# Optimization experiments

Hardware: AMD Instinct MI355X
Metric: run time of the kernel (lower is better)

Reference implementation:

```python
import jax, jax.numpy as jnp
import numpy as np

N_NODES = 50000


def gcn_conv(x, edge_index, W, b, n_nodes):
    # Linear transform first (as in PyG GCNConv), then normalized aggregation
    xw = x @ W  # [N, out]
    src, dst = edge_index[0], edge_index[1]
    loops = jnp.arange(n_nodes, dtype=src.dtype)
    s = jnp.concatenate([src, loops])  # add self-loops
    d = jnp.concatenate([dst, loops])
    deg = jax.ops.segment_sum(jnp.ones_like(s, dtype=xw.dtype), d, num_segments=n_nodes)
    dinv = jnp.where(deg > 0, jax.lax.rsqrt(deg), 0.0)
    norm = dinv[s] * dinv[d]  # [E+N]
    msg = xw[s] * norm[:, None]  # gather + scale
    out = jax.ops.segment_sum(msg, d, num_segments=n_nodes)  # scatter-add
    return out + b


def setup_inputs() -> dict:
    key = jax.random.key(0)
    k1, k2, k3, k4 = jax.random.split(key, 4)
    in_dim, hidden = 128, 128
    n_edges = 625000
    x = jax.random.normal(k1, (N_NODES, in_dim), dtype=jnp.float32)
    edge_index = jax.random.randint(k2, (2, n_edges), 0, N_NODES, dtype=jnp.int64)
    # glorot-ish scale
    W1 = jax.random.normal(k3, (in_dim, hidden), dtype=jnp.float32) * (1.0 / np.sqrt(in_dim))
    b1 = jnp.zeros((hidden,), dtype=jnp.float32)
    W2 = jax.random.normal(k4, (hidden, hidden), dtype=jnp.float32) * (1.0 / np.sqrt(hidden))
    b2 = jnp.zeros((hidden,), dtype=jnp.float32)
    return {"x": x, "edge_index": edge_index, "W1": W1, "b1": b1, "W2": W2, "b2": b2}


def reference(x, edge_index, W1, b1, W2, b2):
    n = x.shape[0]
    h = gcn_conv(x, edge_index, W1, b1, n)
    h = jax.nn.relu(h)
    # dropout(p=0.3) is identity in eval mode
    h = gcn_conv(h, edge_index, W2, b2, n)
    return jax.nn.relu(h)
```

## Files before the change

### kernel.cpp

```cpp
#include <hip/hip_runtime.h>
#include <hip/hip_bf16.h>

#define NNODES 50000
#define BKT 64
#define LP 136

typedef short bf16x8 __attribute__((ext_vector_type(8)));
typedef float f32x4 __attribute__((ext_vector_type(4)));

__device__ __forceinline__ unsigned short f2bf_rn(float f) {
    unsigned int u = __float_as_uint(f);
    return (unsigned short)((u + 0x7fffu + ((u >> 16) & 1u)) >> 16);
}
__device__ __forceinline__ float bf_lo(unsigned int u) { return __uint_as_float(u << 16); }
__device__ __forceinline__ float bf_hi(unsigned int u) { return __uint_as_float(u & 0xffff0000u); }

__device__ __forceinline__ void acc8(float* a, uint4 u, float wv) {
    a[0] = fmaf(bf_lo(u.x), wv, a[0]);  a[1] = fmaf(bf_hi(u.x), wv, a[1]);
    a[2] = fmaf(bf_lo(u.y), wv, a[2]);  a[3] = fmaf(bf_hi(u.y), wv, a[3]);
    a[4] = fmaf(bf_lo(u.z), wv, a[4]);  a[5] = fmaf(bf_hi(u.z), wv, a[5]);
    a[6] = fmaf(bf_lo(u.w), wv, a[6]);  a[7] = fmaf(bf_hi(u.w), wv, a[7]);
}


__global__ __launch_bounds__(256) void k_wt(const float* __restrict__ W1,
                                            const float* __restrict__ W2,
                                            unsigned short* __restrict__ WT1,
                                            unsigned short* __restrict__ WT2,
                                            int* __restrict__ cnt, int N) {
    __shared__ float tile[128 * 129];
    int b = blockIdx.x, t = threadIdx.x;
    if (b < 2) {
        const float* W = b ? W2 : W1;
        unsigned short* WT = b ? WT2 : WT1;
        for (int idx = t; idx < 128 * 128; idx += 256)
            tile[(idx >> 7) * 129 + (idx & 127)] = W[idx];
        __syncthreads();
        for (int idx = t; idx < 128 * 128; idx += 256) {
            int c = idx >> 7, k = idx & 127;
            WT[c * 128 + k] = f2bf_rn(tile[k * 129 + c]);
        }
    } else {
        int i = (b - 2) * 256 + t;
        if (i < N) cnt[i] = 0;
    }
}


__global__ __launch_bounds__(256) void k_gemmbucket(const float* __restrict__ X,
                                                    const unsigned short* __restrict__ WT,
                                                    unsigned short* __restrict__ Yb, int n,
                                                    const int* __restrict__ src,
                                                    const int* __restrict__ dst,
                                                    int* __restrict__ cnt,
                                                    unsigned short* __restrict__ bkt,
                                                    int E, int EB) {
    __shared__ unsigned short Wl[128 * LP];
    int t = threadIdx.x;
    if ((int)blockIdx.x < EB) {
        int e = blockIdx.x * 256 + t;
        if (e < E) {
            int s = src[e], d = dst[e];
            int pos = atomicAdd(&cnt[d], 1);
            if (pos < BKT) bkt[(size_t)d * BKT + pos] = (unsigned short)s;
        }
        return;
    }
    int gb = blockIdx.x - EB;
    int lane = t & 63, w = t >> 6;
    int m = lane & 15, quad = lane >> 4;
    int base = gb * 64 + w * 16;
    int row = min(base + m, n - 1);

    bf16x8 a[4];
#pragma unroll
    for (int kt = 0; kt < 4; ++kt) {
        const float* pa = &X[(size_t)row * 128 + kt * 32 + quad * 8];
        float4 v0 = *(const float4*)pa;
        float4 v1 = *(const float4*)(pa + 4);
        a[kt][0] = (short)f2bf_rn(v0.x); a[kt][1] = (short)f2bf_rn(v0.y);
        a[kt][2] = (short)f2bf_rn(v0.z); a[kt][3] = (short)f2bf_rn(v0.w);
        a[kt][4] = (short)f2bf_rn(v1.x); a[kt][5] = (short)f2bf_rn(v1.y);
        a[kt][6] = (short)f2bf_rn(v1.z); a[kt][7] = (short)f2bf_rn(v1.w);
    }
    for (int idx = t; idx < 128 * 16; idx += 256) {
        int r = idx >> 4, c8 = (idx & 15) << 3;
        *(uint4*)&Wl[r * LP + c8] = *(const uint4*)&WT[r * 128 + c8];
    }
    __syncthreads();

    f32x4 acc[8];
#pragma unroll
    for (int i = 0; i < 8; ++i) acc[i] = f32x4{0.f, 0.f, 0.f, 0.f};
#pragma unroll
    for (int kt = 0; kt < 4; ++kt) {
        int ko = kt * 32 + quad * 8;
#pragma unroll
        for (int ct = 0; ct < 8; ++ct) {
            bf16x8 bb = *(const bf16x8*)&Wl[(ct * 16 + m) * LP + ko];
            acc[ct] = __builtin_amdgcn_mfma_f32_16x16x32_bf16(a[kt], bb, acc[ct], 0, 0, 0);
        }
    }
    __syncthreads();

    unsigned short* ep = &Wl[w * 16 * LP];
#pragma unroll
    for (int ct = 0; ct < 8; ++ct)
#pragma unroll
        for (int r = 0; r < 4; ++r)
            ep[(quad * 4 + r) * LP + ct * 16 + m] = f2bf_rn(acc[ct][r]);
    __syncthreads();
    int rr = lane & 15, cc = lane >> 4;
    int orow = base + rr;
    if (orow < n) {
#pragma unroll
        for (int i2 = 0; i2 < 4; ++i2)
            ((uint4*)&Yb[(size_t)orow * 128])[cc * 4 + i2] =
                *(const uint4*)&ep[rr * LP + (cc * 4 + i2) * 8];
    }
}


__global__ __launch_bounds__(1024, 2) void k_aggemm(const unsigned int* __restrict__ xw1u,
                                                    const int* __restrict__ cnt,
                                                    const unsigned short* __restrict__ bkt,
                                                    const float* __restrict__ bias,
                                                    const unsigned short* __restrict__ WT2,
                                                    unsigned short* __restrict__ xw2, int n) {
    __shared__ unsigned short Wl[128 * LP];
    __shared__ unsigned short At[64 * LP];
    int t = threadIdx.x, lane = t & 63, w = t >> 6;
    int base = blockIdx.x * 64;

    for (int idx = t; idx < 128 * 16; idx += 1024) {
        int r = idx >> 4, c8 = (idx & 15) << 3;
        *(uint4*)&Wl[r * LP + c8] = *(const uint4*)&WT2[r * 128 + c8];
    }

    int g = lane >> 4, li = lane & 15;
    int node = min(base + w * 4 + g, n - 1);
    int deg = cnt[node], degc = min(deg, BKT);
    float di = rsqrtf((float)deg + 1.0f);
    uint4 v = *(const uint4*)&xw1u[(size_t)node * 64 + li * 4];
    float a[8];
    a[0] = di * bf_lo(v.x);  a[1] = di * bf_hi(v.x);
    a[2] = di * bf_lo(v.y);  a[3] = di * bf_hi(v.y);
    a[4] = di * bf_lo(v.z);  a[5] = di * bf_hi(v.z);
    a[6] = di * bf_lo(v.w);  a[7] = di * bf_hi(v.w);
    const unsigned short* bp = &bkt[(size_t)node * BKT];
    for (int j = 0; __any(j < degc); j += 8) {
        if (j < degc) {
            uint4 q = *(const uint4*)&bp[j];
            int s0 = q.x & 0xffff, s1 = q.x >> 16, s2 = q.y & 0xffff, s3 = q.y >> 16;
            int s4 = q.z & 0xffff, s5 = q.z >> 16, s6 = q.w & 0xffff, s7 = q.w >> 16;
            uint4 u0 = *(const uint4*)&xw1u[(size_t)s0 * 64 + li * 4];
            uint4 u1 = *(const uint4*)&xw1u[(size_t)s1 * 64 + li * 4];
            uint4 u2 = *(const uint4*)&xw1u[(size_t)s2 * 64 + li * 4];
            uint4 u3 = *(const uint4*)&xw1u[(size_t)s3 * 64 + li * 4];
            uint4 u4 = *(const uint4*)&xw1u[(size_t)s4 * 64 + li * 4];
            uint4 u5 = *(const uint4*)&xw1u[(size_t)s5 * 64 + li * 4];
            uint4 u6 = *(const uint4*)&xw1u[(size_t)s6 * 64 + li * 4];
            uint4 u7 = *(const uint4*)&xw1u[(size_t)s7 * 64 + li * 4];
            float w0 = (j + 0 < degc) ? rsqrtf((float)cnt[s0] + 1.0f) : 0.0f;
            float w1 = (j + 1 < degc) ? rsqrtf((float)cnt[s1] + 1.0f) : 0.0f;
            float w2 = (j + 2 < degc) ? rsqrtf((float)cnt[s2] + 1.0f) : 0.0f;
            float w3 = (j + 3 < degc) ? rsqrtf((float)cnt[s3] + 1.0f) : 0.0f;
            float w4 = (j + 4 < degc) ? rsqrtf((float)cnt[s4] + 1.0f) : 0.0f;
            float w5 = (j + 5 < degc) ? rsqrtf((float)cnt[s5] + 1.0f) : 0.0f;
            float w6 = (j + 6 < degc) ? rsqrtf((float)cnt[s6] + 1.0f) : 0.0f;
            float w7 = (j + 7 < degc) ? rsqrtf((float)cnt[s7] + 1.0f) : 0.0f;
            acc8(a, u0, w0); acc8(a, u1, w1); acc8(a, u2, w2); acc8(a, u3, w3);
            acc8(a, u4, w4); acc8(a, u5, w5); acc8(a, u6, w6); acc8(a, u7, w7);
        }
    }
    float4 b0 = ((const float4*)bias)[li * 2];
    float4 b1v = ((const float4*)bias)[li * 2 + 1];
    float h0 = fmaxf(fmaf(di, a[0], b0.x), 0.f), h1 = fmaxf(fmaf(di, a[1], b0.y), 0.f);
    float h2 = fmaxf(fmaf(di, a[2], b0.z), 0.f), h3 = fmaxf(fmaf(di, a[3], b0.w), 0.f);
    float h4 = fmaxf(fmaf(di, a[4], b1v.x), 0.f), h5 = fmaxf(fmaf(di, a[5], b1v.y), 0.f);
    float h6 = fmaxf(fmaf(di, a[6], b1v.z), 0.f), h7 = fmaxf(fmaf(di, a[7], b1v.w), 0.f);
    uint4 hp;
    hp.x = (unsigned)f2bf_rn(h0) | ((unsigned)f2bf_rn(h1) << 16);
    hp.y = (unsigned)f2bf_rn(h2) | ((unsigned)f2bf_rn(h3) << 16);
    hp.z = (unsigned)f2bf_rn(h4) | ((unsigned)f2bf_rn(h5) << 16);
    hp.w = (unsigned)f2bf_rn(h6) | ((unsigned)f2bf_rn(h7) << 16);
    *(uint4*)&At[(w * 4 + g) * LP + li * 8] = hp;

    int m = lane & 15, quad = lane >> 4;
    int ct = w & 7, mt2 = (w >> 3) * 2;
    float die[2][4];
#pragma unroll
    for (int mt = 0; mt < 2; ++mt)
#pragma unroll
        for (int r = 0; r < 4; ++r)
            die[mt][r] = rsqrtf(
                (float)cnt[min(base + (mt2 + mt) * 16 + quad * 4 + r, n - 1)] + 1.0f);
    __syncthreads();

    f32x4 acc0 = f32x4{0.f, 0.f, 0.f, 0.f};
    f32x4 acc1 = f32x4{0.f, 0.f, 0.f, 0.f};
#pragma unroll
    for (int kt = 0; kt < 4; ++kt) {
        int ko = kt * 32 + quad * 8;
        bf16x8 bb = *(const bf16x8*)&Wl[(ct * 16 + m) * LP + ko];
        bf16x8 aA = *(const bf16x8*)&At[(mt2 * 16 + m) * LP + ko];
        bf16x8 aB = *(const bf16x8*)&At[((mt2 + 1) * 16 + m) * LP + ko];
        acc0 = __builtin_amdgcn_mfma_f32_16x16x32_bf16(aA, bb, acc0, 0, 0, 0);
        acc1 = __builtin_amdgcn_mfma_f32_16x16x32_bf16(aB, bb, acc1, 0, 0, 0);
    }
    __syncthreads();
#pragma unroll
    for (int r = 0; r < 4; ++r) {
        At[(mt2 * 16 + quad * 4 + r) * LP + ct * 16 + m] = f2bf_rn(acc0[r] * die[0][r]);
        At[((mt2 + 1) * 16 + quad * 4 + r) * LP + ct * 16 + m] = f2bf_rn(acc1[r] * die[1][r]);
    }
    __syncthreads();
    {
        int rowi = t >> 4, q = t & 15;
        int orow = base + rowi;
        if (orow < n)
            *(uint4*)&xw2[(size_t)orow * 128 + q * 8] = *(const uint4*)&At[rowi * LP + q * 8];
    }
}


__global__ __launch_bounds__(256) void k_agg(const unsigned int* __restrict__ xw2u,
                                             const int* __restrict__ cnt,
                                             const unsigned short* __restrict__ bkt,
                                             const float* __restrict__ bias,
                                             float* __restrict__ out, int n) {
    int t = threadIdx.x, lane = t & 63, w = t >> 6;
    int g = lane >> 4, li = lane & 15;
    int node = blockIdx.x * 16 + w * 4 + g;
    int nc = min(node, n - 1);
    int deg = cnt[nc], degc = min(deg, BKT);
    float di = rsqrtf((float)deg + 1.0f);
    uint4 v = *(const uint4*)&xw2u[(size_t)nc * 64 + li * 4];
    float a[8];
    a[0] = bf_lo(v.x);  a[1] = bf_hi(v.x);
    a[2] = bf_lo(v.y);  a[3] = bf_hi(v.y);
    a[4] = bf_lo(v.z);  a[5] = bf_hi(v.z);
    a[6] = bf_lo(v.w);  a[7] = bf_hi(v.w);
    const unsigned short* bp = &bkt[(size_t)nc * BKT];
    for (int j = 0; __any(j < degc); j += 8) {
        if (j < degc) {
            uint4 q = *(const uint4*)&bp[j];
            int s0 = q.x & 0xffff, s1 = q.x >> 16, s2 = q.y & 0xffff, s3 = q.y >> 16;
            int s4 = q.z & 0xffff, s5 = q.z >> 16, s6 = q.w & 0xffff, s7 = q.w >> 16;
            uint4 u0 = *(const uint4*)&xw2u[(size_t)s0 * 64 + li * 4];
            uint4 u1 = *(const uint4*)&xw2u[(size_t)s1 * 64 + li * 4];
            uint4 u2 = *(const uint4*)&xw2u[(size_t)s2 * 64 + li * 4];
            uint4 u3 = *(const uint4*)&xw2u[(size_t)s3 * 64 + li * 4];
            uint4 u4 = *(const uint4*)&xw2u[(size_t)s4 * 64 + li * 4];
            uint4 u5 = *(const uint4*)&xw2u[(size_t)s5 * 64 + li * 4];
            uint4 u6 = *(const uint4*)&xw2u[(size_t)s6 * 64 + li * 4];
            uint4 u7 = *(const uint4*)&xw2u[(size_t)s7 * 64 + li * 4];
            float w0 = (j + 0 < degc) ? 1.0f : 0.0f, w1 = (j + 1 < degc) ? 1.0f : 0.0f;
            float w2 = (j + 2 < degc) ? 1.0f : 0.0f, w3 = (j + 3 < degc) ? 1.0f : 0.0f;
            float w4 = (j + 4 < degc) ? 1.0f : 0.0f, w5 = (j + 5 < degc) ? 1.0f : 0.0f;
            float w6 = (j + 6 < degc) ? 1.0f : 0.0f, w7 = (j + 7 < degc) ? 1.0f : 0.0f;
            acc8(a, u0, w0); acc8(a, u1, w1); acc8(a, u2, w2); acc8(a, u3, w3);
            acc8(a, u4, w4); acc8(a, u5, w5); acc8(a, u6, w6); acc8(a, u7, w7);
        }
    }
    float4 b0 = ((const float4*)bias)[li * 2];
    float4 b1v = ((const float4*)bias)[li * 2 + 1];
    float4 o0, o1;
    o0.x = fmaxf(fmaf(di, a[0], b0.x), 0.f);  o0.y = fmaxf(fmaf(di, a[1], b0.y), 0.f);
    o0.z = fmaxf(fmaf(di, a[2], b0.z), 0.f);  o0.w = fmaxf(fmaf(di, a[3], b0.w), 0.f);
    o1.x = fmaxf(fmaf(di, a[4], b1v.x), 0.f); o1.y = fmaxf(fmaf(di, a[5], b1v.y), 0.f);
    o1.z = fmaxf(fmaf(di, a[6], b1v.z), 0.f); o1.w = fmaxf(fmaf(di, a[7], b1v.w), 0.f);
    if (node < n) {
        *(float4*)&out[(size_t)node * 128 + li * 8] = o0;
        *(float4*)&out[(size_t)node * 128 + li * 8 + 4] = o1;
    }
}


extern "C" void kernel_launch(void* const* d_in, const int* in_sizes, int n_in,
                              void* d_out, int out_size, void* d_ws, size_t ws_size,
                              hipStream_t stream) {
    const float* x  = (const float*)d_in[0];
    const int*   ei = (const int*)d_in[1];
    const float* W1 = (const float*)d_in[2];
    const float* b1 = (const float*)d_in[3];
    const float* W2 = (const float*)d_in[4];
    const float* b2 = (const float*)d_in[5];
    float* out = (float*)d_out;

    const int N = NNODES;
    const int E = in_sizes[1] / 2;
    const int* src = ei;
    const int* dst = ei + E;

    char* p = (char*)d_ws;
    size_t off = 0;
    auto take = [&](size_t bytes) -> void* {
        void* r = p + off;
        off = (off + bytes + 255) & ~(size_t)255;
        return r;
    };
    int* cnt = (int*)take((size_t)N * 4);
    unsigned short* bkt = (unsigned short*)take((size_t)N * BKT * 2);
    unsigned short* w1t = (unsigned short*)take(128 * 128 * 2);
    unsigned short* w2t = (unsigned short*)take(128 * 128 * 2);
    unsigned short* xw1 = (unsigned short*)take((size_t)N * 128 * 2);
    unsigned short* xw2 = (unsigned short*)take((size_t)N * 128 * 2);

    const int NB = (N + 255) / 256;
    const int EB = (E + 255) / 256;
    const int GB = (N + 63) / 64;
    const int AB = (N + 15) / 16;

    k_wt<<<2 + NB, 256, 0, stream>>>(W1, W2, w1t, w2t, cnt, N);
    k_gemmbucket<<<EB + GB, 256, 0, stream>>>(x, w1t, xw1, N, src, dst, cnt, bkt, E, EB);
    k_aggemm<<<GB, 1024, 0, stream>>>((const unsigned int*)xw1, cnt, bkt, b1, w2t, xw2, N);
    k_agg<<<AB, 256, 0, stream>>>((const unsigned int*)xw2, cnt, bkt, b2, out, N);
}
```

Before: 209.5 us.

## Shard edge bucketing per XCD and compact buckets with precomputed dinv

Edge bucketing now writes into eight per-XCD sub-buckets indexed by the hardware XCC_ID, so atomics on a node's counter stay within one die's L2 and avoid cross-die contention. A new compaction kernel merges the sub-buckets into the per-node bucket and precomputes the inverse square-root degree once per node. The aggregation kernels then read dinv directly instead of recomputing rsqrt from counts. This adds a kernel launch, a larger zero-init, and extra memory traffic for the 8x counter and bucket arrays.

After: 209.1 us. Within noise of the previous version (-0.2%).

```diff
diff --git a/kernel.cpp b/kernel.cpp
--- a/kernel.cpp
+++ b/kernel.cpp
@@ -3,6 +3,7 @@
 
 #define NNODES 50000
 #define BKT 64
+#define CAP8 32
 #define LP 136
 
 typedef short bf16x8 __attribute__((ext_vector_type(8)));
@@ -27,7 +28,7 @@
                                             const float* __restrict__ W2,
                                             unsigned short* __restrict__ WT1,
                                             unsigned short* __restrict__ WT2,
-                                            int* __restrict__ cnt, int N) {
+                                            int* __restrict__ cnt8, int N8) {
     __shared__ float tile[128 * 129];
     int b = blockIdx.x, t = threadIdx.x;
     if (b < 2) {
@@ -42,7 +43,7 @@
         }
     } else {
         int i = (b - 2) * 256 + t;
-        if (i < N) cnt[i] = 0;
+        if (i < N8) cnt8[i] = 0;
     }
 }
 
@@ -52,17 +53,21 @@
                                                     unsigned short* __restrict__ Yb, int n,
                                                     const int* __restrict__ src,
                                                     const int* __restrict__ dst,
-                                                    int* __restrict__ cnt,
-                                                    unsigned short* __restrict__ bkt,
+                                                    int* __restrict__ cnt8,
+                                                    unsigned short* __restrict__ bkt8,
                                                     int E, int EB) {
     __shared__ unsigned short Wl[128 * LP];
     int t = threadIdx.x;
     if ((int)blockIdx.x < EB) {
+        unsigned int xcd;
+        asm("s_getreg_b32 %0, hwreg(HW_REG_XCC_ID)" : "=s"(xcd));
+        xcd &= 7;
         int e = blockIdx.x * 256 + t;
         if (e < E) {
             int s = src[e], d = dst[e];
-            int pos = atomicAdd(&cnt[d], 1);
-            if (pos < BKT) bkt[(size_t)d * BKT + pos] = (unsigned short)s;
+            int pos = atomicAdd(&cnt8[xcd * n + d], 1);
+            if (pos < CAP8)
+                bkt8[((size_t)xcd * n + d) * CAP8 + pos] = (unsigned short)s;
         }
         return;
     }
@@ -121,8 +126,44 @@
 }
 
 
+__global__ __launch_bounds__(256) void k_compact(const int* __restrict__ cnt8,
+                                                 const unsigned short* __restrict__ bkt8,
+                                                 int* __restrict__ cnt,
+                                                 float* __restrict__ dinvf,
+                                                 unsigned short* __restrict__ bkt, int N) {
+    __shared__ int scnt[32][8];
+    int t = threadIdx.x;
+    int nn = t >> 3, x = t & 7;
+    int node = blockIdx.x * 32 + nn;
+    int nc = min(node, N - 1);
+    int c = cnt8[x * N + nc];
+    scnt[nn][x] = c;
+    __syncthreads();
+    int off = 0, ent = 0, traw = 0;
+#pragma unroll
+    for (int k = 0; k < 8; ++k) {
+        int v = scnt[nn][k];
+        int vc = min(v, CAP8);
+        if (k < x) off += vc;
+        ent += vc;
+        traw += v;
+    }
+    if (node < N) {
+        if (x == 0) {
+            cnt[node] = min(ent, BKT);
+            dinvf[node] = rsqrtf((float)traw + 1.0f);
+        }
+        int cc = min(c, CAP8);
+        const unsigned short* sp = &bkt8[((size_t)x * N + nc) * CAP8];
+        unsigned short* dp = &bkt[(size_t)node * BKT];
+        for (int j = 0; j < cc && off + j < BKT; ++j) dp[off + j] = sp[j];
+    }
+}
+
+
 __global__ __launch_bounds__(1024, 2) void k_aggemm(const unsigned int* __restrict__ xw1u,
                                                     const int* __restrict__ cnt,
+                                                    const float* __restrict__ dinvf,
                                                     const unsigned short* __restrict__ bkt,
                                                     const float* __restrict__ bias,
                                                     const unsigned short* __restrict__ WT2,
@@ -139,8 +180,8 @@
 
     int g = lane >> 4, li = lane & 15;
     int node = min(base + w * 4 + g, n - 1);
-    int deg = cnt[node], degc = min(deg, BKT);
-    float di = rsqrtf((float)deg + 1.0f);
+    int degc = cnt[node];
+    float di = dinvf[node];
     uint4 v = *(const uint4*)&xw1u[(size_t)node * 64 + li * 4];
     float a[8];
     a[0] = di * bf_lo(v.x);  a[1] = di * bf_hi(v.x);
@@ -161,14 +202,14 @@
             uint4 u5 = *(const uint4*)&xw1u[(size_t)s5 * 64 + li * 4];
             uint4 u6 = *(const uint4*)&xw1u[(size_t)s6 * 64 + li * 4];
             uint4 u7 = *(const uint4*)&xw1u[(size_t)s7 * 64 + li * 4];
-            float w0 = (j + 0 < degc) ? rsqrtf((float)cnt[s0] + 1.0f) : 0.0f;
-            float w1 = (j + 1 < degc) ? rsqrtf((float)cnt[s1] + 1.0f) : 0.0f;
-            float w2 = (j + 2 < degc) ? rsqrtf((float)cnt[s2] + 1.0f) : 0.0f;
-            float w3 = (j + 3 < degc) ? rsqrtf((float)cnt[s3] + 1.0f) : 0.0f;
-            float w4 = (j + 4 < degc) ? rsqrtf((float)cnt[s4] + 1.0f) : 0.0f;
-            float w5 = (j + 5 < degc) ? rsqrtf((float)cnt[s5] + 1.0f) : 0.0f;
-            float w6 = (j + 6 < degc) ? rsqrtf((float)cnt[s6] + 1.0f) : 0.0f;
-            float w7 = (j + 7 < degc) ? rsqrtf((float)cnt[s7] + 1.0f) : 0.0f;
+            float w0 = (j + 0 < degc) ? dinvf[s0] : 0.0f;
+            float w1 = (j + 1 < degc) ? dinvf[s1] : 0.0f;
+            float w2 = (j + 2 < degc) ? dinvf[s2] : 0.0f;
+            float w3 = (j + 3 < degc) ? dinvf[s3] : 0.0f;
+            float w4 = (j + 4 < degc) ? dinvf[s4] : 0.0f;
+            float w5 = (j + 5 < degc) ? dinvf[s5] : 0.0f;
+            float w6 = (j + 6 < degc) ? dinvf[s6] : 0.0f;
+            float w7 = (j + 7 < degc) ? dinvf[s7] : 0.0f;
             acc8(a, u0, w0); acc8(a, u1, w1); acc8(a, u2, w2); acc8(a, u3, w3);
             acc8(a, u4, w4); acc8(a, u5, w5); acc8(a, u6, w6); acc8(a, u7, w7);
         }
@@ -193,8 +234,7 @@
     for (int mt = 0; mt < 2; ++mt)
 #pragma unroll
         for (int r = 0; r < 4; ++r)
-            die[mt][r] = rsqrtf(
-                (float)cnt[min(base + (mt2 + mt) * 16 + quad * 4 + r, n - 1)] + 1.0f);
+            die[mt][r] = dinvf[min(base + (mt2 + mt) * 16 + quad * 4 + r, n - 1)];
     __syncthreads();
 
     f32x4 acc0 = f32x4{0.f, 0.f, 0.f, 0.f};
@@ -226,6 +266,7 @@
 
 __global__ __launch_bounds__(256) void k_agg(const unsigned int* __restrict__ xw2u,
                                              const int* __restrict__ cnt,
+                                             const float* __restrict__ dinvf,
                                              const unsigned short* __restrict__ bkt,
                                              const float* __restrict__ bias,
                                              float* __restrict__ out, int n) {
@@ -233,8 +274,8 @@
     int g = lane >> 4, li = lane & 15;
     int node = blockIdx.x * 16 + w * 4 + g;
     int nc = min(node, n - 1);
-    int deg = cnt[nc], degc = min(deg, BKT);
-    float di = rsqrtf((float)deg + 1.0f);
+    int degc = cnt[nc];
+    float di = dinvf[nc];
     uint4 v = *(const uint4*)&xw2u[(size_t)nc * 64 + li * 4];
     float a[8];
     a[0] = bf_lo(v.x);  a[1] = bf_hi(v.x);
@@ -300,20 +341,26 @@
         off = (off + bytes + 255) & ~(size_t)255;
         return r;
     };
+    int* cnt8 = (int*)take((size_t)8 * N * 4);
+    unsigned short* bkt8 = (unsigned short*)take((size_t)8 * N * CAP8 * 2);
     int* cnt = (int*)take((size_t)N * 4);
+    float* dinvf = (float*)take((size_t)N * 4);
     unsigned short* bkt = (unsigned short*)take((size_t)N * BKT * 2);
     unsigned short* w1t = (unsigned short*)take(128 * 128 * 2);
     unsigned short* w2t = (unsigned short*)take(128 * 128 * 2);
     unsigned short* xw1 = (unsigned short*)take((size_t)N * 128 * 2);
     unsigned short* xw2 = (unsigned short*)take((size_t)N * 128 * 2);
 
-    const int NB = (N + 255) / 256;
+    const int NZ = (8 * N + 255) / 256;
     const int EB = (E + 255) / 256;
     const int GB = (N + 63) / 64;
+    const int CB = (N + 31) / 32;
     const int AB = (N + 15) / 16;
 
-    k_wt<<<2 + NB, 256, 0, stream>>>(W1, W2, w1t, w2t, cnt, N);
-    k_gemmbucket<<<EB + GB, 256, 0, stream>>>(x, w1t, xw1, N, src, dst, cnt, bkt, E, EB);
-    k_aggemm<<<GB, 1024, 0, stream>>>((const unsigned int*)xw1, cnt, bkt, b1, w2t, xw2, N);
-    k_agg<<<AB, 256, 0, stream>>>((const unsigned int*)xw2, cnt, bkt, b2, out, N);
-}
+    k_wt<<<2 + NZ, 256, 0, stream>>>(W1, W2, w1t, w2t, cnt8, 8 * N);
+    k_gemmbucket<<<EB + GB, 256, 0, stream>>>(x, w1t, xw1, N, src, dst, cnt8, bkt8, E, EB);
+    k_compact<<<CB, 256, 0, stream>>>(cnt8, bkt8, cnt, dinvf, bkt, N);
+    k_aggemm<<<GB, 1024, 0, stream>>>((const unsigned int*)xw1, cnt, dinvf, bkt,
+                                      b1, w2t, xw2, N);
+    k_agg<<<AB, 256, 0, stream>>>((const unsigned int*)xw2, cnt, dinvf, bkt, b2, out, N);
+}
```
